# Kernel tuning notes

Measured on AMD Instinct MI355X. Metric: run time of the kernel, lower is better.

Reference implementation:

```python
import jax, jax.numpy as jnp
import numpy as np

B, N, IN_DIM, H, L = 8, 1024, 3, 256, 3
NUM_STEPS = 200
LN_EPS = 1e-5


def _cdist(a, b):
    # Euclidean pairwise distance, a:[B,n,d], b:[B,m,d] -> [B,n,m]
    d2 = (jnp.sum(a * a, -1)[:, :, None] + jnp.sum(b * b, -1)[:, None, :]
          - 2.0 * jnp.einsum('bik,bjk->bij', a, b))
    d2 = jnp.maximum(d2, 0.0)
    safe = jnp.sqrt(jnp.where(d2 > 0, d2, 1.0))
    return jnp.where(d2 > 0, safe, 0.0)


def _layernorm(x, g, b):
    mu = jnp.mean(x, -1, keepdims=True)
    var = jnp.mean(jnp.square(x - mu), -1, keepdims=True)
    return (x - mu) * jax.lax.rsqrt(var + LN_EPS) * g + b


def setup_inputs() -> dict:
    key = jax.random.key(0)
    ks = jax.random.split(key, 32)
    s = 0.02
    inp = {
        'x': jax.random.normal(ks[0], (B, N, IN_DIM), jnp.float32),
        't': jax.random.randint(ks[1], (B,), 0, NUM_STEPS),
        'mask': jnp.ones((B, N), bool),
        # top-level weights (stored [in,out])
        'w_time': jax.random.normal(ks[2], (1, H)) * s,
        'b_time': jnp.zeros((H,)),
        'w_in': jax.random.normal(ks[3], (IN_DIM + H, H)) * s,
        'b_in': jnp.zeros((H,)),
        'w_out': jax.random.normal(ks[4], (H, IN_DIM)) * s,
        'b_out': jnp.zeros((IN_DIM,)),
        # per-layer stacked params [L, ...]
        'qkv_w': jax.random.normal(ks[5], (L, H, 3 * H)) * s,
        'qkv_b': jnp.zeros((L, 3 * H)),
        'ao_w': jax.random.normal(ks[6], (L, H, H)) * s,
        'ao_b': jnp.zeros((L, H)),
        'fc1_w': jax.random.normal(ks[7], (L, H, 4 * H)) * s,
        'fc1_b': jax.random.normal(ks[8], (L, 4 * H)) * s,
        'fc2_w': jax.random.normal(ks[9], (L, 4 * H, H)) * s,
        'fc2_b': jax.random.normal(ks[10], (L, H)) * s,
        'ln1_g': jnp.ones((L, H)), 'ln1_b': jnp.zeros((L, H)),
        'ln2_g': jnp.ones((L, H)), 'ln2_b': jnp.zeros((L, H)),
    }
    return inp


def reference(x, t, mask, w_time, b_time, w_in, b_in, w_out, b_out,
              qkv_w, qkv_b, ao_w, ao_b, fc1_w, fc1_b, fc2_w, fc2_b,
              ln1_g, ln1_b, ln2_g, ln2_b):
    tf = t.astype(jnp.float32)[:, None] / float(NUM_STEPS)          # [B,1]
    t_embed = jax.nn.relu(tf @ w_time + b_time)                      # [B,H]
    t_embed = jnp.broadcast_to(t_embed[:, None, :], (B, N, H))
    h = jax.nn.relu(jnp.concatenate([x, t_embed], -1) @ w_in + b_in)  # [B,N,H]
    geo = _cdist(h[:, :, :3], h[:, :, :3])                           # [B,N,N]
    mask_f = mask.astype(h.dtype)
    scale = 1.0 / jnp.sqrt(jnp.float32(H))
    for l in range(L):
        qkv = (h @ qkv_w[l] + qkv_b[l]).reshape(B, N, 3, H)
        q, k, v = qkv[:, :, 0], qkv[:, :, 1], qkv[:, :, 2]
        dist = _cdist(geo, geo)                                      # cdist of the distance matrix itself
        scores = jnp.einsum('bik,bjk->bij', q, k) * scale * jnp.exp(-dist)
        scores = jnp.where(mask[:, None, :], scores, -jnp.inf)
        attn = jax.nn.softmax(scores, axis=-1)
        ao = (jnp.einsum('bij,bjk->bik', attn, v) @ ao_w[l] + ao_b[l]) * mask_f[:, :, None]
        xx = _layernorm(h + ao, ln1_g[l], ln1_b[l])
        f1 = jax.nn.relu((xx @ fc1_w[l] + fc1_b[l]) * mask_f[:, :, None])
        ffn = jax.nn.relu((f1 @ fc2_w[l] + fc2_b[l]) * mask_f[:, :, None])
        h = _layernorm(xx + ffn, ln2_g[l], ln2_b[l])
    return (h @ w_out + b_out) * mask_f[:, :, None]
```

## Files before the change

### kernel.cpp

```cpp
#include <hip/hip_runtime.h>
#include <math.h>

#define NB 8
#define NN 1024
#define NH 256
#define NL 3

typedef unsigned short u16;
typedef __bf16 bf16x8 __attribute__((ext_vector_type(8)));
typedef float f32x4 __attribute__((ext_vector_type(4)));

constexpr int EPI_BIAS_RELU = 2, EPI_BIAS_RELU_RESID = 3,
              EPI_BIAS_RESID = 4, EPI_EDIST = 5, EPI_QKV = 6;

__device__ __forceinline__ unsigned bf16rne(float f) {
    unsigned u = __float_as_uint(f);
    return (u + 0x7fffu + ((u >> 16) & 1u)) >> 16;
}
__device__ __forceinline__ unsigned bfpair(float a, float b) {
    return bf16rne(a) | (bf16rne(b) << 16);
}
__device__ __forceinline__ float bf2f(u16 h) {
    unsigned u = ((unsigned)h) << 16;
    return __uint_as_float(u);
}

__device__ __forceinline__ float blockSum256(float v) {
    __shared__ float sm[4];
    #pragma unroll
    for (int o = 32; o; o >>= 1) v += __shfl_down(v, o, 64);
    int lane = threadIdx.x & 63, wid = threadIdx.x >> 6;
    if (lane == 0) sm[wid] = v;
    __syncthreads();
    if (threadIdx.x == 0) sm[0] = sm[0] + sm[1] + sm[2] + sm[3];
    __syncthreads();
    float r = sm[0];
    __syncthreads();
    return r;
}

template <int EPI, bool AUG, bool OBF, int SWZ, int MT>
__global__ __launch_bounds__(256) void gemm_mfma(
    const u16* __restrict__ A, int lda, long sA,
    const u16* __restrict__ Bt, int ldb, long sB,
    void* __restrict__ C, int ldc, long sC,
    int K,
    const float* __restrict__ bias, long sBias,
    const float* __restrict__ resid, int ldr,
    u16* __restrict__ vtout)
{
    constexpr int MF = MT / 32;
    constexpr int ASZ = MT * 8;
    __shared__ uint4 sm4[ASZ + 1024];
    const int tid = threadIdx.x;

    int bx = blockIdx.x, by = blockIdx.y, bz = blockIdx.z;
    bool trans = false;
    if (SWZ == 2) {
        int gx = gridDim.x;
        int T = gx * gridDim.y;
        int lid = bx + gx * by;
        int nl = (lid & 7) * (T >> 3) + (lid >> 3);
        bx = nl % gx; by = nl / gx;
    } else if (SWZ == 3) {
        int lid = bx + gridDim.x * bz;
        bz = lid & 7;
        int idx = lid >> 3;
        int j = 0;
        while (idx >= 16 - 2 * j) { idx -= 16 - 2 * j; j++; }
        by = 2 * j + idx;
        bx = j;
        trans = (by >= 2 * bx + 2);
    }
    const int z = bz;
    const int row0 = by * MT, col0 = bx * 128;

    f32x4 acc[MF][4];
    #pragma unroll
    for (int m = 0; m < MF; m++)
        #pragma unroll
        for (int n = 0; n < 4; n++) acc[m][n] = (f32x4){0.f, 0.f, 0.f, 0.f};

    const int l = tid & 63, wid = tid >> 6;
    const int wr = wid >> 1, wc = wid & 1;
    const int lrow = l & 15, lgrp = l >> 4;

    for (int k0 = 0; k0 < K; k0 += 64) {
        int kk = k0, aOff = 0, bOff = 0;
        if (AUG) {
            int seg = k0 >> 10;
            kk = k0 & 1023;
            aOff = (seg == 2) ? 1024 : 0;
            bOff = (seg == 1) ? 1024 : 0;
        }
        if (MT == 128) {
            const int srow = tid >> 1, half = tid & 1, cb = half * 4, swz = srow & 7;
            const u16* Ap = A + (long)z * sA + (long)(row0 + srow) * lda + kk + aOff + half * 32;
            uint4 a0 = *(const uint4*)(Ap + 0),  a1 = *(const uint4*)(Ap + 8);
            uint4 a2 = *(const uint4*)(Ap + 16), a3 = *(const uint4*)(Ap + 24);
            sm4[srow * 8 + ((cb + 0) ^ swz)] = a0;
            sm4[srow * 8 + ((cb + 1) ^ swz)] = a1;
            sm4[srow * 8 + ((cb + 2) ^ swz)] = a2;
            sm4[srow * 8 + ((cb + 3) ^ swz)] = a3;
        } else {
            const int arow = tid >> 2, aq = tid & 3, swz = arow & 7;
            const u16* Ap = A + (long)z * sA + (long)(row0 + arow) * lda + kk + aOff + aq * 16;
            uint4 a0 = *(const uint4*)(Ap + 0), a1 = *(const uint4*)(Ap + 8);
            sm4[arow * 8 + ((aq * 2 + 0) ^ swz)] = a0;
            sm4[arow * 8 + ((aq * 2 + 1) ^ swz)] = a1;
        }
        {
            const int brow = tid >> 1, bq = tid & 1, cb = bq * 4, swz = brow & 7;
            const u16* Bp = Bt + (long)z * sB + (long)(col0 + brow) * ldb + kk + bOff + bq * 32;
            uint4 b0 = *(const uint4*)(Bp + 0),  b1 = *(const uint4*)(Bp + 8);
            uint4 b2 = *(const uint4*)(Bp + 16), b3 = *(const uint4*)(Bp + 24);
            sm4[ASZ + brow * 8 + ((cb + 0) ^ swz)] = b0;
            sm4[ASZ + brow * 8 + ((cb + 1) ^ swz)] = b1;
            sm4[ASZ + brow * 8 + ((cb + 2) ^ swz)] = b2;
            sm4[ASZ + brow * 8 + ((cb + 3) ^ swz)] = b3;
        }
        __syncthreads();

        #pragma unroll
        for (int ks = 0; ks < 2; ks++) {
            int c = ks * 4 + lgrp;
            bf16x8 a[MF], b[4];
            #pragma unroll
            for (int m = 0; m < MF; m++) {
                int r = wr * (MT / 2) + m * 16 + lrow;
                a[m] = __builtin_bit_cast(bf16x8, sm4[r * 8 + (c ^ (r & 7))]);
            }
            #pragma unroll
            for (int n = 0; n < 4; n++) {
                int r = wc * 64 + n * 16 + lrow;
                b[n] = __builtin_bit_cast(bf16x8, sm4[ASZ + r * 8 + (c ^ (r & 7))]);
            }
            #pragma unroll
            for (int m = 0; m < MF; m++)
                #pragma unroll
                for (int n = 0; n < 4; n++)
                    acc[m][n] = __builtin_amdgcn_mfma_f32_16x16x32_bf16(a[m], b[n], acc[m][n], 0, 0, 0);
        }
        __syncthreads();
    }

    #pragma unroll
    for (int m = 0; m < MF; m++) {
        #pragma unroll
        for (int n = 0; n < 4; n++) {
            int rbase = row0 + wr * (MT / 2) + m * 16 + lgrp * 4;
            int cc = col0 + wc * 64 + n * 16 + lrow;
            float bv = 0.f;
            if (EPI == EPI_QKV || EPI == EPI_BIAS_RELU || EPI == EPI_BIAS_RELU_RESID || EPI == EPI_BIAS_RESID)
                bv = bias[cc];
            float vals[4];
            #pragma unroll
            for (int reg = 0; reg < 4; reg++) {
                long r = rbase + reg;
                float v = acc[m][n][reg];
                if (EPI == EPI_QKV) v += bv;
                else if (EPI == EPI_BIAS_RELU) v = fmaxf(v + bv, 0.f);
                else if (EPI == EPI_BIAS_RELU_RESID) v = fmaxf(v + bv, 0.f) + resid[r * ldr + cc];
                else if (EPI == EPI_BIAS_RESID) v = v + bv + resid[r * ldr + cc];
                else if (EPI == EPI_EDIST) {
                    const float* rnb = bias + (long)z * sBias;
                    float d2 = fmaxf(rnb[r] + rnb[cc] - 2.f * v, 0.f);
                    v = expf(-sqrtf(d2));
                }
                vals[reg] = v;
                if (OBF) ((u16*)C)[(long)z * sC + r * ldc + cc] = (u16)bf16rne(v);
                else     ((float*)C)[(long)z * sC + r * ldc + cc] = v;
            }
            if (EPI == EPI_EDIST && SWZ == 3 && trans) {
                uint2 tv;
                tv.x = bfpair(vals[0], vals[1]);
                tv.y = bfpair(vals[2], vals[3]);
                *(uint2*)&((u16*)C)[(long)z * sC + (long)cc * ldc + rbase] = tv;
            }
            if (EPI == EPI_QKV && cc >= 512) {
                int b = rbase >> 10;
                uint2 tv;
                tv.x = bfpair(vals[0], vals[1]);
                tv.y = bfpair(vals[2], vals[3]);
                *(uint2*)&vtout[(long)b * NH * NN + (long)(cc - 512) * NN + (rbase & 1023)] = tv;
            }
        }
    }
}

__global__ __launch_bounds__(512) void flash_k(
    const u16* __restrict__ qkv,
    const u16* __restrict__ vt,
    const u16* __restrict__ edist,
    u16* __restrict__ obuf,
    float scale)
{
    __shared__ uint4 Ks[128][32];
    __shared__ uint4 Vts[256][16];
    __shared__ __align__(16) u16 Es[32][136];
    __shared__ __align__(16) u16 Ps[32][136];
    __shared__ float rs[32][8];

    const int tid = threadIdx.x;
    const int l = tid & 63, w = tid >> 6;
    const int g = l >> 4, lr = l & 15;

    int lid = blockIdx.x + gridDim.x * blockIdx.y;
    const int b = lid & 7;
    const int q0 = (lid >> 3) * 32;

    const u16* qkvb = qkv + (long)b * NN * 768;
    const u16* vtb  = vt + (long)b * NH * NN;
    const u16* eb   = edist + (long)b * NN * NN;

    uint4 qf[2][8];
    #pragma unroll
    for (int m = 0; m < 2; m++)
        #pragma unroll
        for (int ks = 0; ks < 8; ks++)
            qf[m][ks] = *(const uint4*)(qkvb + (long)(q0 + 16 * m + lr) * 768 + 32 * ks + 8 * g);

    f32x4 oacc[2][2];
    #pragma unroll
    for (int m = 0; m < 2; m++)
        #pragma unroll
        for (int nf = 0; nf < 2; nf++) oacc[m][nf] = (f32x4){0.f, 0.f, 0.f, 0.f};
    float rsum[2][4] = {{0.f, 0.f, 0.f, 0.f}, {0.f, 0.f, 0.f, 0.f}};

    for (int n0 = 0; n0 < NN; n0 += 128) {
        #pragma unroll
        for (int i = 0; i < 8; i++) {
            int idx = tid + 512 * i;
            int row = idx >> 5, ch = idx & 31;
            Ks[row][ch ^ (row & 7)] = *(const uint4*)(qkvb + (long)(n0 + row) * 768 + 256 + ch * 8);
        }
        #pragma unroll
        for (int i = 0; i < 8; i++) {
            int idx = tid + 512 * i;
            int c = idx >> 4, ch = idx & 15;
            Vts[c][(ch & 8) | ((ch & 7) ^ (c & 7))] = *(const uint4*)(vtb + (long)c * NN + n0 + ch * 8);
        }
        {
            int r = tid >> 4, ch = tid & 15;
            *(uint4*)&Es[r][ch * 8] = *(const uint4*)(eb + (long)(q0 + r) * NN + n0 + ch * 8);
        }
        __syncthreads();

        f32x4 s[2];
        s[0] = (f32x4){0.f, 0.f, 0.f, 0.f};
        s[1] = (f32x4){0.f, 0.f, 0.f, 0.f};
        const int krow = w * 16 + lr;
        #pragma unroll
        for (int ks = 0; ks < 8; ks++) {
            bf16x8 kf = __builtin_bit_cast(bf16x8, Ks[krow][(4 * ks + g) ^ (krow & 7)]);
            s[0] = __builtin_amdgcn_mfma_f32_16x16x32_bf16(__builtin_bit_cast(bf16x8, qf[0][ks]), kf, s[0], 0, 0, 0);
            s[1] = __builtin_amdgcn_mfma_f32_16x16x32_bf16(__builtin_bit_cast(bf16x8, qf[1][ks]), kf, s[1], 0, 0, 0);
        }
        #pragma unroll
        for (int m = 0; m < 2; m++)
            #pragma unroll
            for (int reg = 0; reg < 4; reg++) {
                int q = 16 * m + 4 * g + reg;
                int kc = w * 16 + lr;
                float p = expf(s[m][reg] * scale * bf2f(Es[q][kc]));
                rsum[m][reg] += p;
                Ps[q][kc] = (u16)bf16rne(p);
            }
        __syncthreads();
        #pragma unroll
        for (int ks = 0; ks < 4; ks++) {
            bf16x8 pa[2], vb[2];
            #pragma unroll
            for (int m = 0; m < 2; m++)
                pa[m] = __builtin_bit_cast(bf16x8, *(const uint4*)&Ps[16 * m + lr][32 * ks + 8 * g]);
            #pragma unroll
            for (int nf = 0; nf < 2; nf++) {
                int c = w * 32 + nf * 16 + lr;
                int ch = 4 * ks + g;
                vb[nf] = __builtin_bit_cast(bf16x8, Vts[c][(ch & 8) | ((ch & 7) ^ (c & 7))]);
            }
            #pragma unroll
            for (int m = 0; m < 2; m++)
                #pragma unroll
                for (int nf = 0; nf < 2; nf++)
                    oacc[m][nf] = __builtin_amdgcn_mfma_f32_16x16x32_bf16(pa[m], vb[nf], oacc[m][nf], 0, 0, 0);
        }
        __syncthreads();
    }

    #pragma unroll
    for (int m = 0; m < 2; m++)
        #pragma unroll
        for (int reg = 0; reg < 4; reg++) {
            float v = rsum[m][reg];
            v += __shfl_xor(v, 1); v += __shfl_xor(v, 2);
            v += __shfl_xor(v, 4); v += __shfl_xor(v, 8);
            rsum[m][reg] = v;
        }
    if (lr == 0) {
        #pragma unroll
        for (int m = 0; m < 2; m++)
            #pragma unroll
            for (int reg = 0; reg < 4; reg++)
                rs[16 * m + 4 * g + reg][w] = rsum[m][reg];
    }
    __syncthreads();
    #pragma unroll
    for (int m = 0; m < 2; m++) {
        #pragma unroll
        for (int reg = 0; reg < 4; reg++) {
            int q = 16 * m + 4 * g + reg;
            float t = 0.f;
            #pragma unroll
            for (int j = 0; j < 8; j++) t += rs[q][j];
            float inv = 1.f / t;
            #pragma unroll
            for (int nf = 0; nf < 2; nf++) {
                int c = w * 32 + nf * 16 + lr;
                obuf[(long)b * NN * NH + (long)(q0 + q) * NH + c] = (u16)bf16rne(oacc[m][nf][reg] * inv);
            }
        }
    }
}

__global__ __launch_bounds__(256) void base_k(const int* __restrict__ t,
                                              const float* __restrict__ w_time,
                                              const float* __restrict__ b_time,
                                              const float* __restrict__ w_in,
                                              const float* __restrict__ b_in,
                                              float* __restrict__ base) {
    int b = blockIdx.x, j = threadIdx.x;
    __shared__ float te[256];
    float tf = (float)t[b] / 200.0f;
    te[j] = fmaxf(tf * w_time[j] + b_time[j], 0.f);
    __syncthreads();
    float acc = b_in[j];
    for (int k = 0; k < 256; k++) acc = fmaf(te[k], w_in[(3 + k) * 256 + j], acc);
    base[b * 256 + j] = acc;
}

__global__ __launch_bounds__(256) void hinit_k(const float* __restrict__ x,
                                               const float* __restrict__ w_in,
                                               const float* __restrict__ base,
                                               float* __restrict__ h,
                                               u16* __restrict__ hbf,
                                               float* __restrict__ h3) {
    long row = blockIdx.x;
    int b = (int)(row >> 10);
    int j = threadIdx.x;
    float x0 = x[row * 3 + 0], x1 = x[row * 3 + 1], x2 = x[row * 3 + 2];
    float v = base[b * 256 + j];
    v = fmaf(x0, w_in[j], v);
    v = fmaf(x1, w_in[256 + j], v);
    v = fmaf(x2, w_in[512 + j], v);
    v = fmaxf(v, 0.f);
    h[row * 256 + j] = v;
    hbf[row * 256 + j] = (u16)bf16rne(v);
    if (j < 3) h3[row * 3 + j] = v;
}

__global__ __launch_bounds__(256) void geo_k(const float* __restrict__ h3,
                                             u16* __restrict__ ghl,
                                             float* __restrict__ rn) {
    int bi = blockIdx.x;
    int b = bi >> 10, i = bi & 1023;
    const float* hb = h3 + (long)b * NN * 3;
    float ax = hb[i * 3 + 0], ay = hb[i * 3 + 1], az = hb[i * 3 + 2];
    u16* grow = ghl + (long)bi * 2048;
    float accs = 0.f;
    #pragma unroll
    for (int j0 = 0; j0 < NN; j0 += 256) {
        int j = j0 + threadIdx.x;
        float dx = hb[j * 3 + 0] - ax, dy = hb[j * 3 + 1] - ay, dz = hb[j * 3 + 2] - az;
        float d2 = dx * dx + dy * dy + dz * dz;
        float d = (d2 > 0.f) ? sqrtf(d2) : 0.f;
        u16 hi = (u16)bf16rne(d);
        float fhi = bf2f(hi);
        u16 lo = (u16)bf16rne(d - fhi);
        float rep = fhi + bf2f(lo);
        grow[j] = hi;
        grow[1024 + j] = lo;
        accs += rep * rep;
    }
    float tot = blockSum256(accs);
    if (threadIdx.x == 0) rn[bi] = tot;
}

__global__ __launch_bounds__(256) void wtrans_k(const float* __restrict__ qkv_w,
                                                const float* __restrict__ ao_w,
                                                const float* __restrict__ fc1_w,
                                                const float* __restrict__ fc2_w,
                                                u16* __restrict__ qkv_wt,
                                                u16* __restrict__ ao_wt,
                                                u16* __restrict__ fc1_wt,
                                                u16* __restrict__ fc2_wt) {
    int type = blockIdx.z, lyr = blockIdx.y;
    int R, Cc;
    const float* src;
    u16* dst;
    if (type == 0) { R = 256; Cc = 768;  src = qkv_w + (long)lyr * R * Cc; dst = qkv_wt + (long)lyr * R * Cc; }
    else if (type == 1) { R = 256; Cc = 256; src = ao_w + (long)lyr * R * Cc; dst = ao_wt + (long)lyr * R * Cc; }
    else if (type == 2) { R = 256; Cc = 1024; src = fc1_w + (long)lyr * R * Cc; dst = fc1_wt + (long)lyr * R * Cc; }
    else { R = 1024; Cc = 256; src = fc2_w + (long)lyr * R * Cc; dst = fc2_wt + (long)lyr * R * Cc; }
    int tC = Cc >> 5, tR = R >> 5;
    int tile = blockIdx.x;
    if (tile >= tC * tR) return;
    int c0 = (tile % tC) << 5, r0 = (tile / tC) << 5;
    __shared__ float tf[32][33];
    int tx = threadIdx.x & 31, ty = threadIdx.x >> 5;
    #pragma unroll
    for (int i = 0; i < 4; i++) {
        int r = ty + 8 * i;
        tf[r][tx] = src[(long)(r0 + r) * Cc + c0 + tx];
    }
    __syncthreads();
    #pragma unroll
    for (int i = 0; i < 4; i++) {
        int c = ty + 8 * i;
        dst[(long)(c0 + c) * R + r0 + tx] = (u16)bf16rne(tf[tx][c]);
    }
}

__global__ __launch_bounds__(256) void ln_k(float* __restrict__ X,
                                            u16* __restrict__ Xbf,
                                            const float* __restrict__ g,
                                            const float* __restrict__ b) {
    int wid = threadIdx.x >> 6, l = threadIdx.x & 63;
    long row = (long)blockIdx.x * 4 + wid;
    float* p = X + row * NH;
    float4 v = *(float4*)(p + l * 4);
    float s = v.x + v.y + v.z + v.w;
    #pragma unroll
    for (int o = 32; o; o >>= 1) s += __shfl_xor(s, o);
    float mu = s * (1.f / NH);
    float4 d = {v.x - mu, v.y - mu, v.z - mu, v.w - mu};
    float q = d.x * d.x + d.y * d.y + d.z * d.z + d.w * d.w;
    #pragma unroll
    for (int o = 32; o; o >>= 1) q += __shfl_xor(q, o);
    float rsd = rsqrtf(q * (1.f / NH) + 1e-5f);
    float4 g4 = *(const float4*)(g + l * 4);
    float4 b4 = *(const float4*)(b + l * 4);
    float4 o4;
    o4.x = d.x * rsd * g4.x + b4.x;
    o4.y = d.y * rsd * g4.y + b4.y;
    o4.z = d.z * rsd * g4.z + b4.z;
    o4.w = d.w * rsd * g4.w + b4.w;
    *(float4*)(p + l * 4) = o4;
    uint2 pk;
    pk.x = bfpair(o4.x, o4.y);
    pk.y = bfpair(o4.z, o4.w);
    *(uint2*)(Xbf + row * NH + l * 4) = pk;
}

__global__ __launch_bounds__(256) void out_k(const float* __restrict__ h,
                                             const float* __restrict__ w_out,
                                             const float* __restrict__ b_out,
                                             float* __restrict__ out) {
    long row = blockIdx.x;
    int wid = threadIdx.x >> 6, lane = threadIdx.x & 63;
    if (wid < 3) {
        float acc = 0.f;
        for (int k = lane; k < 256; k += 64) acc = fmaf(h[row * 256 + k], w_out[k * 3 + wid], acc);
        #pragma unroll
        for (int o = 32; o; o >>= 1) acc += __shfl_down(acc, o, 64);
        if (lane == 0) out[row * 3 + wid] = acc + b_out[wid];
    }
}

extern "C" void kernel_launch(void* const* d_in, const int* in_sizes, int n_in,
                              void* d_out, int out_size, void* d_ws, size_t ws_size,
                              hipStream_t stream) {
    const float* x      = (const float*)d_in[0];
    const int*   t      = (const int*)  d_in[1];
    const float* w_time = (const float*)d_in[3];
    const float* b_time = (const float*)d_in[4];
    const float* w_in   = (const float*)d_in[5];
    const float* b_in   = (const float*)d_in[6];
    const float* w_out  = (const float*)d_in[7];
    const float* b_out  = (const float*)d_in[8];
    const float* qkv_w  = (const float*)d_in[9];
    const float* qkv_b  = (const float*)d_in[10];
    const float* ao_w   = (const float*)d_in[11];
    const float* ao_b   = (const float*)d_in[12];
    const float* fc1_w  = (const float*)d_in[13];
    const float* fc1_b  = (const float*)d_in[14];
    const float* fc2_w  = (const float*)d_in[15];
    const float* fc2_b  = (const float*)d_in[16];
    const float* ln1_g  = (const float*)d_in[17];
    const float* ln1_b  = (const float*)d_in[18];
    const float* ln2_g  = (const float*)d_in[19];
    const float* ln2_b  = (const float*)d_in[20];
    float* out = (float*)d_out;

    char* W = (char*)d_ws;
    float* h     = (float*)(W);
    float* xb    = (float*)(W + (8ul << 20));
    u16*   obuf  = (u16*)  (W + (16ul << 20));
    u16*   hbf   = (u16*)  (W + (20ul << 20));
    u16*   xbbf  = (u16*)  (W + (24ul << 20));
    u16*   vt    = (u16*)  (W + (28ul << 20));
    u16*   f1    = (u16*)  (W + (32ul << 20));
    u16*   qkvb  = (u16*)  (W + (48ul << 20));
    u16*   edist = (u16*)  (W + (60ul << 20));
    u16*   ghl   = (u16*)  (W + (76ul << 20));
    u16*   wts   = (u16*)  (W + (108ul << 20));
    u16* qkv_wt = wts;
    u16* ao_wt  = wts + 589824;
    u16* fc1_wt = wts + 786432;
    u16* fc2_wt = wts + 1572864;
    float* base = (float*)(W + (114ul << 20));
    float* rn   = base + 2048;
    float* h3   = rn + 8192;

    const float scale = 1.0f / 16.0f;

    base_k<<<NB, 256, 0, stream>>>(t, w_time, b_time, w_in, b_in, base);
    hinit_k<<<NB * NN, 256, 0, stream>>>(x, w_in, base, h, hbf, h3);
    geo_k<<<NB * NN, 256, 0, stream>>>(h3, ghl, rn);
    wtrans_k<<<dim3(256, NL, 4), 256, 0, stream>>>(qkv_w, ao_w, fc1_w, fc2_w,
                                                   qkv_wt, ao_wt, fc1_wt, fc2_wt);
    gemm_mfma<EPI_EDIST, true, true, 3, 64><<<dim3(72, 1, 8), 256, 0, stream>>>(
        ghl, 2048, (long)NN * 2048, ghl, 2048, (long)NN * 2048,
        edist, NN, (long)NN * NN, 3072, rn, NN, nullptr, 0, nullptr);

    for (int l = 0; l < NL; ++l) {
        gemm_mfma<EPI_QKV, false, true, 2, 128><<<dim3(6, 64, 1), 256, 0, stream>>>(
            hbf, NH, 0, qkv_wt + (long)l * 196608, NH, 0, qkvb, 768, 0,
            NH, qkv_b + l * 768, 0, nullptr, 0, vt);
        flash_k<<<dim3(32, 8), 512, 0, stream>>>(qkvb, vt, edist, obuf, scale);
        gemm_mfma<EPI_BIAS_RESID, false, false, 2, 64><<<dim3(2, 128, 1), 256, 0, stream>>>(
            obuf, NH, 0, ao_wt + (long)l * 65536, NH, 0, xb, NH, 0,
            NH, ao_b + l * NH, 0, h, NH, nullptr);
        ln_k<<<2048, 256, 0, stream>>>(xb, xbbf, ln1_g + l * NH, ln1_b + l * NH);
        gemm_mfma<EPI_BIAS_RELU, false, true, 2, 128><<<dim3(8, 64, 1), 256, 0, stream>>>(
            xbbf, NH, 0, fc1_wt + (long)l * 262144, NH, 0, f1, 1024, 0,
            NH, fc1_b + l * 1024, 0, nullptr, 0, nullptr);
        gemm_mfma<EPI_BIAS_RELU_RESID, false, false, 2, 64><<<dim3(2, 128, 1), 256, 0, stream>>>(
            f1, 1024, 0, fc2_wt + (long)l * 262144, 1024, 0, h, NH, 0,
            1024, fc2_b + l * NH, 0, xb, NH, nullptr);
        ln_k<<<2048, 256, 0, stream>>>(h, hbf, ln2_g + l * NH, ln2_b + l * NH);
    }
    out_k<<<NB * NN, 256, 0, stream>>>(h, w_out, b_out, out);
}
```

Baseline: 381.4 us.

## Fuse attention output projection and LayerNorm into flash kernel; fp16 single-pass edist

The flash attention kernel now stages its normalized output in shared memory, multiplies it by the attention-output weight with MFMA, adds bias and residual, and applies LayerNorm1 in place. This removes the separate output-projection GEMM and LN launches and the obuf round trip through memory. Separately, the geometry distance matrix is stored as a single fp16 operand instead of a bf16 hi/lo split, which cuts the edist GEMM's K from 3072 to 1024. The diagonal is forced to exactly 1 to absorb the rounding error. Precision of the distance-of-distances drops to fp16, and the fused kernel reads the projection weights from global memory in every block.

```diff
diff --git a/kernel.cpp b/kernel.cpp
--- a/kernel.cpp
+++ b/kernel.cpp
@@ -8,10 +8,10 @@
 
 typedef unsigned short u16;
 typedef __bf16 bf16x8 __attribute__((ext_vector_type(8)));
+typedef _Float16 f16x8 __attribute__((ext_vector_type(8)));
 typedef float f32x4 __attribute__((ext_vector_type(4)));
 
-constexpr int EPI_BIAS_RELU = 2, EPI_BIAS_RELU_RESID = 3,
-              EPI_BIAS_RESID = 4, EPI_EDIST = 5, EPI_QKV = 6;
+constexpr int EPI_BIAS_RELU = 2, EPI_BIAS_RELU_RESID = 3, EPI_EDIST = 5, EPI_QKV = 6;
 
 __device__ __forceinline__ unsigned bf16rne(float f) {
     unsigned u = __float_as_uint(f);
@@ -39,7 +39,7 @@
     return r;
 }
 
-template <int EPI, bool AUG, bool OBF, int SWZ, int MT>
+template <int EPI, int DT, bool OBF, int SWZ, int MT>
 __global__ __launch_bounds__(256) void gemm_mfma(
     const u16* __restrict__ A, int lda, long sA,
     const u16* __restrict__ Bt, int ldb, long sB,
@@ -86,16 +86,9 @@
     const int lrow = l & 15, lgrp = l >> 4;
 
     for (int k0 = 0; k0 < K; k0 += 64) {
-        int kk = k0, aOff = 0, bOff = 0;
-        if (AUG) {
-            int seg = k0 >> 10;
-            kk = k0 & 1023;
-            aOff = (seg == 2) ? 1024 : 0;
-            bOff = (seg == 1) ? 1024 : 0;
-        }
         if (MT == 128) {
             const int srow = tid >> 1, half = tid & 1, cb = half * 4, swz = srow & 7;
-            const u16* Ap = A + (long)z * sA + (long)(row0 + srow) * lda + kk + aOff + half * 32;
+            const u16* Ap = A + (long)z * sA + (long)(row0 + srow) * lda + k0 + half * 32;
             uint4 a0 = *(const uint4*)(Ap + 0),  a1 = *(const uint4*)(Ap + 8);
             uint4 a2 = *(const uint4*)(Ap + 16), a3 = *(const uint4*)(Ap + 24);
             sm4[srow * 8 + ((cb + 0) ^ swz)] = a0;
@@ -104,14 +97,14 @@
             sm4[srow * 8 + ((cb + 3) ^ swz)] = a3;
         } else {
             const int arow = tid >> 2, aq = tid & 3, swz = arow & 7;
-            const u16* Ap = A + (long)z * sA + (long)(row0 + arow) * lda + kk + aOff + aq * 16;
+            const u16* Ap = A + (long)z * sA + (long)(row0 + arow) * lda + k0 + aq * 16;
             uint4 a0 = *(const uint4*)(Ap + 0), a1 = *(const uint4*)(Ap + 8);
             sm4[arow * 8 + ((aq * 2 + 0) ^ swz)] = a0;
             sm4[arow * 8 + ((aq * 2 + 1) ^ swz)] = a1;
         }
         {
             const int brow = tid >> 1, bq = tid & 1, cb = bq * 4, swz = brow & 7;
-            const u16* Bp = Bt + (long)z * sB + (long)(col0 + brow) * ldb + kk + bOff + bq * 32;
+            const u16* Bp = Bt + (long)z * sB + (long)(col0 + brow) * ldb + k0 + bq * 32;
             uint4 b0 = *(const uint4*)(Bp + 0),  b1 = *(const uint4*)(Bp + 8);
             uint4 b2 = *(const uint4*)(Bp + 16), b3 = *(const uint4*)(Bp + 24);
             sm4[ASZ + brow * 8 + ((cb + 0) ^ swz)] = b0;
@@ -124,22 +117,28 @@
         #pragma unroll
         for (int ks = 0; ks < 2; ks++) {
             int c = ks * 4 + lgrp;
-            bf16x8 a[MF], b[4];
+            uint4 a[MF], b[4];
             #pragma unroll
             for (int m = 0; m < MF; m++) {
                 int r = wr * (MT / 2) + m * 16 + lrow;
-                a[m] = __builtin_bit_cast(bf16x8, sm4[r * 8 + (c ^ (r & 7))]);
+                a[m] = sm4[r * 8 + (c ^ (r & 7))];
             }
             #pragma unroll
             for (int n = 0; n < 4; n++) {
                 int r = wc * 64 + n * 16 + lrow;
-                b[n] = __builtin_bit_cast(bf16x8, sm4[ASZ + r * 8 + (c ^ (r & 7))]);
+                b[n] = sm4[ASZ + r * 8 + (c ^ (r & 7))];
             }
             #pragma unroll
             for (int m = 0; m < MF; m++)
                 #pragma unroll
-                for (int n = 0; n < 4; n++)
-                    acc[m][n] = __builtin_amdgcn_mfma_f32_16x16x32_bf16(a[m], b[n], acc[m][n], 0, 0, 0);
+                for (int n = 0; n < 4; n++) {
+                    if (DT == 0)
+                        acc[m][n] = __builtin_amdgcn_mfma_f32_16x16x32_bf16(
+                            __builtin_bit_cast(bf16x8, a[m]), __builtin_bit_cast(bf16x8, b[n]), acc[m][n], 0, 0, 0);
+                    else
+                        acc[m][n] = __builtin_amdgcn_mfma_f32_16x16x32_f16(
+                            __builtin_bit_cast(f16x8, a[m]), __builtin_bit_cast(f16x8, b[n]), acc[m][n], 0, 0, 0);
+                }
         }
         __syncthreads();
     }
@@ -151,7 +150,7 @@
             int rbase = row0 + wr * (MT / 2) + m * 16 + lgrp * 4;
             int cc = col0 + wc * 64 + n * 16 + lrow;
             float bv = 0.f;
-            if (EPI == EPI_QKV || EPI == EPI_BIAS_RELU || EPI == EPI_BIAS_RELU_RESID || EPI == EPI_BIAS_RESID)
+            if (EPI == EPI_QKV || EPI == EPI_BIAS_RELU || EPI == EPI_BIAS_RELU_RESID)
                 bv = bias[cc];
             float vals[4];
             #pragma unroll
@@ -161,11 +160,10 @@
                 if (EPI == EPI_QKV) v += bv;
                 else if (EPI == EPI_BIAS_RELU) v = fmaxf(v + bv, 0.f);
                 else if (EPI == EPI_BIAS_RELU_RESID) v = fmaxf(v + bv, 0.f) + resid[r * ldr + cc];
-                else if (EPI == EPI_BIAS_RESID) v = v + bv + resid[r * ldr + cc];
                 else if (EPI == EPI_EDIST) {
                     const float* rnb = bias + (long)z * sBias;
                     float d2 = fmaxf(rnb[r] + rnb[cc] - 2.f * v, 0.f);
-                    v = expf(-sqrtf(d2));
+                    v = (r == cc) ? 1.f : expf(-sqrtf(d2));
                 }
                 vals[reg] = v;
                 if (OBF) ((u16*)C)[(long)z * sC + r * ldc + cc] = (u16)bf16rne(v);
@@ -192,7 +190,13 @@
     const u16* __restrict__ qkv,
     const u16* __restrict__ vt,
     const u16* __restrict__ edist,
-    u16* __restrict__ obuf,
+    const u16* __restrict__ aow,
+    const float* __restrict__ aob,
+    const float* __restrict__ hres,
+    const float* __restrict__ g1,
+    const float* __restrict__ b1,
+    float* __restrict__ xb,
+    u16* __restrict__ xbbf,
     float scale)
 {
     __shared__ uint4 Ks[128][32];
@@ -200,6 +204,8 @@
     __shared__ __align__(16) u16 Es[32][136];
     __shared__ __align__(16) u16 Ps[32][136];
     __shared__ float rs[32][8];
+    __shared__ float lnA[32][8];
+    __shared__ float lnB[32][8];
 
     const int tid = threadIdx.x;
     const int l = tid & 63, w = tid >> 6;
@@ -269,7 +275,7 @@
         __syncthreads();
         #pragma unroll
         for (int ks = 0; ks < 4; ks++) {
-            bf16x8 pa[2], vb[2];
+            bf16x8 pa[2], vbf[2];
             #pragma unroll
             for (int m = 0; m < 2; m++)
                 pa[m] = __builtin_bit_cast(bf16x8, *(const uint4*)&Ps[16 * m + lr][32 * ks + 8 * g]);
@@ -277,13 +283,13 @@
             for (int nf = 0; nf < 2; nf++) {
                 int c = w * 32 + nf * 16 + lr;
                 int ch = 4 * ks + g;
-                vb[nf] = __builtin_bit_cast(bf16x8, Vts[c][(ch & 8) | ((ch & 7) ^ (c & 7))]);
+                vbf[nf] = __builtin_bit_cast(bf16x8, Vts[c][(ch & 8) | ((ch & 7) ^ (c & 7))]);
             }
             #pragma unroll
             for (int m = 0; m < 2; m++)
                 #pragma unroll
                 for (int nf = 0; nf < 2; nf++)
-                    oacc[m][nf] = __builtin_amdgcn_mfma_f32_16x16x32_bf16(pa[m], vb[nf], oacc[m][nf], 0, 0, 0);
+                    oacc[m][nf] = __builtin_amdgcn_mfma_f32_16x16x32_bf16(pa[m], vbf[nf], oacc[m][nf], 0, 0, 0);
         }
         __syncthreads();
     }
@@ -305,8 +311,10 @@
                 rs[16 * m + 4 * g + reg][w] = rsum[m][reg];
     }
     __syncthreads();
-    #pragma unroll
-    for (int m = 0; m < 2; m++) {
+
+    u16* Os = (u16*)Ks;
+    #pragma unroll
+    for (int m = 0; m < 2; m++)
         #pragma unroll
         for (int reg = 0; reg < 4; reg++) {
             int q = 16 * m + 4 * g + reg;
@@ -317,10 +325,81 @@
             #pragma unroll
             for (int nf = 0; nf < 2; nf++) {
                 int c = w * 32 + nf * 16 + lr;
-                obuf[(long)b * NN * NH + (long)(q0 + q) * NH + c] = (u16)bf16rne(oacc[m][nf][reg] * inv);
-            }
-        }
-    }
+                Os[q * 264 + c] = (u16)bf16rne(oacc[m][nf][reg] * inv);
+            }
+        }
+    __syncthreads();
+
+    f32x4 aacc[2][2];
+    #pragma unroll
+    for (int m = 0; m < 2; m++)
+        #pragma unroll
+        for (int nf = 0; nf < 2; nf++) aacc[m][nf] = (f32x4){0.f, 0.f, 0.f, 0.f};
+    #pragma unroll
+    for (int kc = 0; kc < 8; kc++) {
+        bf16x8 pa[2], wb[2];
+        #pragma unroll
+        for (int m = 0; m < 2; m++)
+            pa[m] = __builtin_bit_cast(bf16x8, *(const uint4*)&Os[(16 * m + lr) * 264 + kc * 32 + 8 * g]);
+        #pragma unroll
+        for (int nf = 0; nf < 2; nf++)
+            wb[nf] = __builtin_bit_cast(bf16x8, *(const uint4*)(aow + (long)(32 * w + 16 * nf + lr) * 256 + kc * 32 + 8 * g));
+        #pragma unroll
+        for (int m = 0; m < 2; m++)
+            #pragma unroll
+            for (int nf = 0; nf < 2; nf++)
+                aacc[m][nf] = __builtin_amdgcn_mfma_f32_16x16x32_bf16(pa[m], wb[nf], aacc[m][nf], 0, 0, 0);
+    }
+
+    int j0 = 32 * w + lr, j1 = 32 * w + 16 + lr;
+    float aob0 = aob[j0], aob1 = aob[j1];
+    float xv[2][2][4];
+    #pragma unroll
+    for (int m = 0; m < 2; m++)
+        #pragma unroll
+        for (int reg = 0; reg < 4; reg++) {
+            int q = 16 * m + 4 * g + reg;
+            long hr = ((long)b * NN + q0 + q) * NH;
+            xv[m][0][reg] = aacc[m][0][reg] + aob0 + hres[hr + j0];
+            xv[m][1][reg] = aacc[m][1][reg] + aob1 + hres[hr + j1];
+        }
+
+    #pragma unroll
+    for (int m = 0; m < 2; m++)
+        #pragma unroll
+        for (int reg = 0; reg < 4; reg++) {
+            float s = xv[m][0][reg] + xv[m][1][reg];
+            float s2 = xv[m][0][reg] * xv[m][0][reg] + xv[m][1][reg] * xv[m][1][reg];
+            s  += __shfl_xor(s, 1);  s  += __shfl_xor(s, 2);  s  += __shfl_xor(s, 4);  s  += __shfl_xor(s, 8);
+            s2 += __shfl_xor(s2, 1); s2 += __shfl_xor(s2, 2); s2 += __shfl_xor(s2, 4); s2 += __shfl_xor(s2, 8);
+            if (lr == 0) {
+                int q = 16 * m + 4 * g + reg;
+                lnA[q][w] = s;
+                lnB[q][w] = s2;
+            }
+        }
+    __syncthreads();
+
+    float g1v0 = g1[j0], g1v1 = g1[j1], b1v0 = b1[j0], b1v1 = b1[j1];
+    #pragma unroll
+    for (int m = 0; m < 2; m++)
+        #pragma unroll
+        for (int reg = 0; reg < 4; reg++) {
+            int q = 16 * m + 4 * g + reg;
+            float S = 0.f, S2 = 0.f;
+            #pragma unroll
+            for (int j = 0; j < 8; j++) { S += lnA[q][j]; S2 += lnB[q][j]; }
+            float mu = S * (1.f / NH);
+            float var = S2 * (1.f / NH) - mu * mu;
+            float rsd = rsqrtf(var + 1e-5f);
+            long hr = ((long)b * NN + q0 + q) * NH;
+            float o0 = (xv[m][0][reg] - mu) * rsd * g1v0 + b1v0;
+            float o1 = (xv[m][1][reg] - mu) * rsd * g1v1 + b1v1;
+            xb[hr + j0] = o0;
+            xb[hr + j1] = o1;
+            xbbf[hr + j0] = (u16)bf16rne(o0);
+            xbbf[hr + j1] = (u16)bf16rne(o1);
+        }
 }
 
 __global__ __launch_bounds__(256) void base_k(const int* __restrict__ t,
@@ -360,13 +439,13 @@
 }
 
 __global__ __launch_bounds__(256) void geo_k(const float* __restrict__ h3,
-                                             u16* __restrict__ ghl,
+                                             u16* __restrict__ gf,
                                              float* __restrict__ rn) {
     int bi = blockIdx.x;
     int b = bi >> 10, i = bi & 1023;
     const float* hb = h3 + (long)b * NN * 3;
     float ax = hb[i * 3 + 0], ay = hb[i * 3 + 1], az = hb[i * 3 + 2];
-    u16* grow = ghl + (long)bi * 2048;
+    u16* grow = gf + (long)bi * 1024;
     float accs = 0.f;
     #pragma unroll
     for (int j0 = 0; j0 < NN; j0 += 256) {
@@ -374,12 +453,9 @@
         float dx = hb[j * 3 + 0] - ax, dy = hb[j * 3 + 1] - ay, dz = hb[j * 3 + 2] - az;
         float d2 = dx * dx + dy * dy + dz * dz;
         float d = (d2 > 0.f) ? sqrtf(d2) : 0.f;
-        u16 hi = (u16)bf16rne(d);
-        float fhi = bf2f(hi);
-        u16 lo = (u16)bf16rne(d - fhi);
-        float rep = fhi + bf2f(lo);
-        grow[j] = hi;
-        grow[1024 + j] = lo;
+        _Float16 hf = (_Float16)d;
+        float rep = (float)hf;
+        grow[j] = __builtin_bit_cast(u16, hf);
         accs += rep * rep;
     }
     float tot = blockSum256(accs);
@@ -495,20 +571,19 @@
     char* W = (char*)d_ws;
     float* h     = (float*)(W);
     float* xb    = (float*)(W + (8ul << 20));
-    u16*   obuf  = (u16*)  (W + (16ul << 20));
-    u16*   hbf   = (u16*)  (W + (20ul << 20));
-    u16*   xbbf  = (u16*)  (W + (24ul << 20));
-    u16*   vt    = (u16*)  (W + (28ul << 20));
-    u16*   f1    = (u16*)  (W + (32ul << 20));
-    u16*   qkvb  = (u16*)  (W + (48ul << 20));
-    u16*   edist = (u16*)  (W + (60ul << 20));
-    u16*   ghl   = (u16*)  (W + (76ul << 20));
-    u16*   wts   = (u16*)  (W + (108ul << 20));
+    u16*   hbf   = (u16*)  (W + (16ul << 20));
+    u16*   xbbf  = (u16*)  (W + (20ul << 20));
+    u16*   vt    = (u16*)  (W + (24ul << 20));
+    u16*   f1    = (u16*)  (W + (28ul << 20));
+    u16*   qkvb  = (u16*)  (W + (44ul << 20));
+    u16*   edist = (u16*)  (W + (56ul << 20));
+    u16*   gf    = (u16*)  (W + (72ul << 20));
+    u16*   wts   = (u16*)  (W + (88ul << 20));
     u16* qkv_wt = wts;
     u16* ao_wt  = wts + 589824;
     u16* fc1_wt = wts + 786432;
     u16* fc2_wt = wts + 1572864;
-    float* base = (float*)(W + (114ul << 20));
+    float* base = (float*)(W + (94ul << 20));
     float* rn   = base + 2048;
     float* h3   = rn + 8192;
 
@@ -516,26 +591,24 @@
 
     base_k<<<NB, 256, 0, stream>>>(t, w_time, b_time, w_in, b_in, base);
     hinit_k<<<NB * NN, 256, 0, stream>>>(x, w_in, base, h, hbf, h3);
-    geo_k<<<NB * NN, 256, 0, stream>>>(h3, ghl, rn);
+    geo_k<<<NB * NN, 256, 0, stream>>>(h3, gf, rn);
     wtrans_k<<<dim3(256, NL, 4), 256, 0, stream>>>(qkv_w, ao_w, fc1_w, fc2_w,
                                                    qkv_wt, ao_wt, fc1_wt, fc2_wt);
-    gemm_mfma<EPI_EDIST, true, true, 3, 64><<<dim3(72, 1, 8), 256, 0, stream>>>(
-        ghl, 2048, (long)NN * 2048, ghl, 2048, (long)NN * 2048,
-        edist, NN, (long)NN * NN, 3072, rn, NN, nullptr, 0, nullptr);
+    gemm_mfma<EPI_EDIST, 1, true, 3, 64><<<dim3(72, 1, 8), 256, 0, stream>>>(
+        gf, 1024, (long)NN * 1024, gf, 1024, (long)NN * 1024,
+        edist, NN, (long)NN * NN, 1024, rn, NN, nullptr, 0, nullptr);
 
     for (int l = 0; l < NL; ++l) {
-        gemm_mfma<EPI_QKV, false, true, 2, 128><<<dim3(6, 64, 1), 256, 0, stream>>>(
+        gemm_mfma<EPI_QKV, 0, true, 2, 128><<<dim3(6, 64, 1), 256, 0, stream>>>(
             hbf, NH, 0, qkv_wt + (long)l * 196608, NH, 0, qkvb, 768, 0,
             NH, qkv_b + l * 768, 0, nullptr, 0, vt);
-        flash_k<<<dim3(32, 8), 512, 0, stream>>>(qkvb, vt, edist, obuf, scale);
-        gemm_mfma<EPI_BIAS_RESID, false, false, 2, 64><<<dim3(2, 128, 1), 256, 0, stream>>>(
-            obuf, NH, 0, ao_wt + (long)l * 65536, NH, 0, xb, NH, 0,
-            NH, ao_b + l * NH, 0, h, NH, nullptr);
-        ln_k<<<2048, 256, 0, stream>>>(xb, xbbf, ln1_g + l * NH, ln1_b + l * NH);
-        gemm_mfma<EPI_BIAS_RELU, false, true, 2, 128><<<dim3(8, 64, 1), 256, 0, stream>>>(
+        flash_k<<<dim3(32, 8), 512, 0, stream>>>(
+            qkvb, vt, edist, ao_wt + (long)l * 65536, ao_b + l * NH,
+            h, ln1_g + l * NH, ln1_b + l * NH, xb, xbbf, scale);
+        gemm_mfma<EPI_BIAS_RELU, 0, true, 2, 128><<<dim3(8, 64, 1), 256, 0, stream>>>(
             xbbf, NH, 0, fc1_wt + (long)l * 262144, NH, 0, f1, 1024, 0,
             NH, fc1_b + l * 1024, 0, nullptr, 0, nullptr);
-        gemm_mfma<EPI_BIAS_RELU_RESID, false, false, 2, 64><<<dim3(2, 128, 1), 256, 0, stream>>>(
+        gemm_mfma<EPI_BIAS_RELU_RESID, 0, false, 2, 64><<<dim3(2, 128, 1), 256, 0, stream>>>(
             f1, 1024, 0, fc2_wt + (long)l * 262144, 1024, 0, h, NH, 0,
             1024, fc2_b + l * NH, 0, xb, NH, nullptr);
         ln_k<<<2048, 256, 0, stream>>>(h, hbf, ln2_g + l * NH, ln2_b + l * NH);
```

After: 330.2 us. 1.16x faster.
